# Kernel tuning notes

Measured on AMD Instinct MI355X. Metric: run time of the kernel, lower is better.

The kernel has to match this reference:

```python
import jax, jax.numpy as jnp
import numpy as np

N = 100000
E = 1600000
IN_C = 128
HID = 256
K_EIG = 64
OUT_C = 16


def setup_inputs() -> dict:
    key = jax.random.key(0)
    ks = jax.random.split(key, 8)
    x = jax.random.normal(ks[0], (N, IN_C), dtype=jnp.float32)
    edge_index = jax.random.randint(ks[1], (2, E), 0, N)
    MLP_W = jax.random.normal(ks[2], (K_EIG, N), dtype=jnp.float32) * 0.02
    MLP_b = jax.random.normal(ks[3], (K_EIG,), dtype=jnp.float32) * 0.02
    mlpx_W = jax.random.normal(ks[4], (HID, IN_C), dtype=jnp.float32) * 0.05
    mlpx_b = jax.random.normal(ks[5], (HID,), dtype=jnp.float32) * 0.02
    fin_W = jax.random.normal(ks[6], (OUT_C, HID + K_EIG), dtype=jnp.float32) * 0.05
    fin_b = jax.random.normal(ks[7], (OUT_C,), dtype=jnp.float32) * 0.02
    return {"x": x, "edge_index": edge_index, "MLP_W": MLP_W, "MLP_b": MLP_b,
            "mlpx_W": mlpx_W, "mlpx_b": mlpx_b, "fin_W": fin_W, "fin_b": fin_b}


def _spmm(row, col, feats, n):
    # adj is COO with coords (col[e], row[e]) and value 1 -> out[col] += feats[row]
    return jax.ops.segment_sum(feats[row], col, num_segments=n)


def _pump(xA, row, col, n):
    # MinCut-style pump: soft assignment, normalized-cut loss + orthogonality loss
    S = jax.nn.softmax(xA, axis=-1)                      # [N, K]
    AS = _spmm(row, col, S, n)                            # A @ S, [N, K]
    cut = jnp.sum(S * AS)                                 # tr(S^T A S)
    deg = jax.ops.segment_sum(jnp.ones(col.shape, S.dtype), col, num_segments=n)
    deg_term = jnp.sum(deg[:, None] * S * S)              # tr(S^T D S)
    pump_loss = -(cut / deg_term)
    SS = S.T @ S                                          # [K, K]
    k = S.shape[1]
    ortho_loss = jnp.linalg.norm(SS / jnp.linalg.norm(SS)
                                 - jnp.eye(k, dtype=S.dtype) / jnp.sqrt(jnp.asarray(k, S.dtype)))
    return S, pump_loss, ortho_loss


def reference(x, edge_index, MLP_W, MLP_b, mlpx_W, mlpx_b, fin_W, fin_b):
    row, col = edge_index[0], edge_index[1]
    n = x.shape[0]
    # xA = adj @ MLP.weight.T + bias   (irregular gather/scatter over edges)
    xA = _spmm(row, col, MLP_W.T, n) + MLP_b              # [N, K]
    xX = x @ mlpx_W.T + mlpx_b                            # [N, HID]
    xA, pump_loss, ortho_loss = _pump(xA, row, col, n)
    z = jnp.concatenate([xX, xA], axis=1)                 # [N, HID+K]
    # dropout omitted (eval mode)
    z = jax.nn.log_softmax(z @ fin_W.T + fin_b, axis=-1)  # [N, OUT]
    return (z, pump_loss + ortho_loss)
```

## Files before the change

### kernel.cpp

```cpp
#include <hip/hip_runtime.h>
#include <math.h>

#define N_NODES 100000
#define N_EDGES 1600000
#define IN_C    128
#define HID     256
#define KEIG    64
#define OUT_C   16

#define NPB      256
#define NBUCKET  ((N_NODES + NPB - 1) / NPB)
#define EDGE_TILE 4096
#define NTILE    ((N_EDGES + EDGE_TILE - 1) / EDGE_TILE)

#define TRANS_BLOCKS   ((N_NODES + 63) / 64)
#define GATHER_BLOCKS  2048
#define CUT_BLOCKS     2048
#define SSP_BLOCKS     512
#define OUT_BLOCKS     ((N_NODES + 255) / 256)

typedef __attribute__((ext_vector_type(8))) short short8;
typedef __attribute__((ext_vector_type(4))) float f32x4;

__device__ __forceinline__ float wave_sum(float v) {
#pragma unroll
    for (int m = 32; m; m >>= 1) v += __shfl_xor(v, m, 64);
    return v;
}
__device__ __forceinline__ float wave_max(float v) {
#pragma unroll
    for (int m = 32; m; m >>= 1) v = fmaxf(v, __shfl_xor(v, m, 64));
    return v;
}
__device__ __forceinline__ float bf2f(unsigned int u) {
    return __uint_as_float((u & 0xffffu) << 16);
}
__device__ __forceinline__ unsigned short f2bf(float f) {
    unsigned int u = __float_as_uint(f);
    u += 0x7fff + ((u >> 16) & 1);
    return (unsigned short)(u >> 16);
}

#define FMA4(P, s, W) \
    P.x = fmaf(s, W.x, P.x); P.y = fmaf(s, W.y, P.y); \
    P.z = fmaf(s, W.z, P.z); P.w = fmaf(s, W.w, P.w);

__global__ void prep_weff(const float* __restrict__ mlpxW, const float* __restrict__ mlpxb,
                          const float* __restrict__ finW, const float* __restrict__ finb,
                          float* __restrict__ Weff, float* __restrict__ beff,
                          int* __restrict__ bcnt) {
    int t = blockIdx.x * blockDim.x + threadIdx.x;
    const int NW = (IN_C + KEIG) * OUT_C;
    if (t < NW) {
        int k = t >> 4, o = t & 15;
        float acc;
        if (k < IN_C) {
            acc = 0.f;
            for (int c = 0; c < HID; ++c)
                acc += mlpxW[c * IN_C + k] * finW[o * (HID + KEIG) + c];
        } else {
            acc = finW[o * (HID + KEIG) + HID + (k - IN_C)];
        }
        Weff[k * OUT_C + o] = acc;
    }
    int tb = t - NW;
    if (tb >= 0 && tb < OUT_C) {
        float acc = finb[tb];
        for (int c = 0; c < HID; ++c) acc += mlpxb[c] * finW[tb * (HID + KEIG) + c];
        beff[tb] = acc;
    }
    int tz = t - (NW + OUT_C);
    if (tz >= 0 && tz <= NBUCKET) bcnt[tz] = 0;
}

__global__ void transpose_w(const float* __restrict__ W, unsigned short* __restrict__ WTb) {
    __shared__ float tile[64][65];
    int n0 = blockIdx.x * 64;
    int t = threadIdx.x;
    int tn = t & 63, tq = t >> 6;
#pragma unroll
    for (int kk = 0; kk < 16; ++kk) {
        int k = tq * 16 + kk;
        int n = n0 + tn;
        tile[k][tn] = (n < N_NODES) ? W[(long long)k * N_NODES + n] : 0.f;
    }
    __syncthreads();
    int tk = t & 63;
#pragma unroll
    for (int ii = 0; ii < 16; ++ii) {
        int n = n0 + tq * 16 + ii;
        if (n < N_NODES) WTb[(long long)n * 64 + tk] = f2bf(tile[tk][tq * 16 + ii]);
    }
}

__global__ void bucket_hist(const int* __restrict__ ei, int* __restrict__ bcnt) {
    __shared__ int h[NBUCKET];
    int t = threadIdx.x;
    for (int i = t; i < NBUCKET; i += 256) h[i] = 0;
    __syncthreads();
    int e0 = blockIdx.x * EDGE_TILE;
    int e1 = min(e0 + EDGE_TILE, N_EDGES);
    for (int e = e0 + t; e < e1; e += 256)
        atomicAdd(&h[ei[N_EDGES + e] >> 8], 1);
    __syncthreads();
    for (int i = t; i < NBUCKET; i += 256)
        if (h[i]) atomicAdd(&bcnt[i], h[i]);
}

__global__ void bucket_scan(const int* __restrict__ bcnt, int* __restrict__ bbase,
                            int* __restrict__ bcur) {
    __shared__ int sh[512];
    int t = threadIdx.x;
    int v = (t < NBUCKET) ? bcnt[t] : 0;
    sh[t] = v;
    __syncthreads();
    for (int d = 1; d < 512; d <<= 1) {
        int u = (t >= d) ? sh[t - d] : 0;
        __syncthreads();
        sh[t] += u;
        __syncthreads();
    }
    if (t < NBUCKET) { bbase[t] = sh[t] - v; bcur[t] = sh[t] - v; }
    if (t == 0) bbase[NBUCKET] = N_EDGES;
}

__global__ void bucket_scatter(const int* __restrict__ ei, int* __restrict__ bcur,
                               int* __restrict__ ebuf) {
    __shared__ int h[NBUCKET];
    __shared__ int gb[NBUCKET];
    int t = threadIdx.x;
    for (int i = t; i < NBUCKET; i += 256) h[i] = 0;
    __syncthreads();
    int e0 = blockIdx.x * EDGE_TILE;
    int e1 = min(e0 + EDGE_TILE, N_EDGES);
    for (int e = e0 + t; e < e1; e += 256)
        atomicAdd(&h[ei[N_EDGES + e] >> 8], 1);
    __syncthreads();
    for (int i = t; i < NBUCKET; i += 256) {
        int c = h[i];
        gb[i] = c ? atomicAdd(&bcur[i], c) : 0;
        h[i] = 0;
    }
    __syncthreads();
    for (int e = e0 + t; e < e1; e += 256) {
        int r = ei[e];
        int c = ei[N_EDGES + e];
        int b = c >> 8;
        int pos = gb[b] + atomicAdd(&h[b], 1);
        ebuf[pos] = r | ((c & 255) << 17);
    }
}

__global__ void csr_build(const int* __restrict__ ebuf, const int* __restrict__ bbase,
                          int* __restrict__ offsets, int* __restrict__ csr_row) {
    __shared__ int hist[NPB];
    __shared__ int sh[NPB];
    __shared__ int curs[NPB];
    int b = blockIdx.x;
    int t = threadIdx.x;
    int s0 = bbase[b], s1 = bbase[b + 1];
    hist[t] = 0;
    __syncthreads();
    for (int i = s0 + t; i < s1; i += 256)
        atomicAdd(&hist[ebuf[i] >> 17], 1);
    __syncthreads();
    int v = hist[t];
    sh[t] = v;
    __syncthreads();
    for (int d = 1; d < 256; d <<= 1) {
        int u = (t >= d) ? sh[t - d] : 0;
        __syncthreads();
        sh[t] += u;
        __syncthreads();
    }
    int excl = s0 + sh[t] - v;
    int node = b * NPB + t;
    if (node < N_NODES) offsets[node] = excl;
    curs[t] = excl;
    __syncthreads();
    for (int i = s0 + t; i < s1; i += 256) {
        int pk = ebuf[i];
        int pos = atomicAdd(&curs[pk >> 17], 1);
        csr_row[pos] = pk & 0x1FFFF;
    }
    if (b == 0 && t == 0) offsets[N_NODES] = N_EDGES;
}

__global__ void gather_softmax(const int* __restrict__ offsets, const int* __restrict__ csr_row,
                               const unsigned short* __restrict__ WTb,
                               const float* __restrict__ MLPb,
                               unsigned short* __restrict__ Sb,
                               float* __restrict__ dtp) {
    int lane = threadIdx.x & 63;
    int wib = threadIdx.x >> 6;
    int gw = (blockIdx.x * blockDim.x + threadIdx.x) >> 6;
    int nw = (gridDim.x * blockDim.x) >> 6;
    float bias = MLPb[lane];
    float dacc = 0.f;
    for (int n = gw; n < N_NODES; n += nw) {
        int s0 = offsets[n], s1 = offsets[n + 1];
        float acc = bias;
        for (int base = s0; base < s1; base += 64) {
            int cnt = min(64, s1 - base);
            int rv = (lane < cnt) ? csr_row[base + lane] : 0;
            int j = 0;
            for (; j + 3 < cnt; j += 4) {
                int r0 = __shfl(rv, j, 64);
                int r1 = __shfl(rv, j + 1, 64);
                int r2 = __shfl(rv, j + 2, 64);
                int r3 = __shfl(rv, j + 3, 64);
                float v0 = bf2f(WTb[(long long)r0 * 64 + lane]);
                float v1 = bf2f(WTb[(long long)r1 * 64 + lane]);
                float v2 = bf2f(WTb[(long long)r2 * 64 + lane]);
                float v3 = bf2f(WTb[(long long)r3 * 64 + lane]);
                acc += (v0 + v1) + (v2 + v3);
            }
            for (; j < cnt; ++j) {
                int r = __shfl(rv, j, 64);
                acc += bf2f(WTb[(long long)r * 64 + lane]);
            }
        }
        float m = wave_max(acc);
        float e = __expf(acc - m);
        float sm = wave_sum(e);
        float sv = e / sm;
        Sb[(long long)n * 64 + lane] = f2bf(sv);
        dacc += (float)(s1 - s0) * sv * sv;
    }
    dacc = wave_sum(dacc);
    __shared__ float red[4];
    if (lane == 0) red[wib] = dacc;
    __syncthreads();
    if (threadIdx.x == 0) dtp[blockIdx.x] = red[0] + red[1] + red[2] + red[3];
}

__global__ void cut_csr(const int* __restrict__ offsets, const int* __restrict__ csr_row,
                        const unsigned short* __restrict__ Sb, float* __restrict__ cutp) {
    int lane = threadIdx.x & 63;
    int wib = threadIdx.x >> 6;
    int gw = (blockIdx.x * blockDim.x + threadIdx.x) >> 6;
    int nw = (gridDim.x * blockDim.x) >> 6;
    float acc = 0.f;
    for (int n = gw; n < N_NODES; n += nw) {
        float sc = bf2f(Sb[(long long)n * 64 + lane]);
        int s0 = offsets[n], s1 = offsets[n + 1];
        float g = 0.f;
        for (int base = s0; base < s1; base += 64) {
            int cnt = min(64, s1 - base);
            int rv = (lane < cnt) ? csr_row[base + lane] : 0;
            int j = 0;
            for (; j + 3 < cnt; j += 4) {
                int r0 = __shfl(rv, j, 64);
                int r1 = __shfl(rv, j + 1, 64);
                int r2 = __shfl(rv, j + 2, 64);
                int r3 = __shfl(rv, j + 3, 64);
                float v0 = bf2f(Sb[(long long)r0 * 64 + lane]);
                float v1 = bf2f(Sb[(long long)r1 * 64 + lane]);
                float v2 = bf2f(Sb[(long long)r2 * 64 + lane]);
                float v3 = bf2f(Sb[(long long)r3 * 64 + lane]);
                g += (v0 + v1) + (v2 + v3);
            }
            for (; j < cnt; ++j) {
                int r = __shfl(rv, j, 64);
                g += bf2f(Sb[(long long)r * 64 + lane]);
            }
        }
        acc += sc * g;
    }
    acc = wave_sum(acc);
    __shared__ float red[4];
    if (lane == 0) red[wib] = acc;
    __syncthreads();
    if (threadIdx.x == 0) cutp[blockIdx.x] = red[0] + red[1] + red[2] + red[3];
}

__global__ __launch_bounds__(256) void ss_mfma(const unsigned short* __restrict__ Sb,
                                               float* __restrict__ ssp) {
    __shared__ unsigned short Sr[32][66];
    int t = threadIdx.x;
    int lane = t & 63;
    int w = t >> 6;
    int m = lane & 15;
    int quad = lane >> 4;
    int srow = t >> 3;
    int spart = t & 7;

    f32x4 a0 = {0.f,0.f,0.f,0.f}, a1 = {0.f,0.f,0.f,0.f};
    f32x4 a2 = {0.f,0.f,0.f,0.f}, a3 = {0.f,0.f,0.f,0.f};

    for (int base = blockIdx.x * 32; base < N_NODES; base += SSP_BLOCKS * 32) {
        const uint4* g = (const uint4*)(Sb + (long long)(base + srow) * 64 + spart * 8);
        uint4 d = *g;
        __syncthreads();
        unsigned int* rowp = (unsigned int*)&Sr[srow][0];
        rowp[spart * 4 + 0] = d.x;
        rowp[spart * 4 + 1] = d.y;
        rowp[spart * 4 + 2] = d.z;
        rowp[spart * 4 + 3] = d.w;
        __syncthreads();

        short8 f0, f1, f2, f3;
#pragma unroll
        for (int j = 0; j < 8; ++j) {
            int k = quad * 8 + j;
            f0[j] = (short)Sr[k][m];
            f1[j] = (short)Sr[k][16 + m];
            f2[j] = (short)Sr[k][32 + m];
            f3[j] = (short)Sr[k][48 + m];
        }
        short8 fa = (w == 0) ? f0 : (w == 1) ? f1 : (w == 2) ? f2 : f3;
        a0 = __builtin_amdgcn_mfma_f32_16x16x32_bf16(fa, f0, a0, 0, 0, 0);
        a1 = __builtin_amdgcn_mfma_f32_16x16x32_bf16(fa, f1, a1, 0, 0, 0);
        a2 = __builtin_amdgcn_mfma_f32_16x16x32_bf16(fa, f2, a2, 0, 0, 0);
        a3 = __builtin_amdgcn_mfma_f32_16x16x32_bf16(fa, f3, a3, 0, 0, 0);
    }

    float* dst = ssp + (size_t)blockIdx.x * 4096;
#pragma unroll
    for (int r = 0; r < 4; ++r) {
        int row = w * 16 + quad * 4 + r;
        dst[row * 64 +  0 + m] = a0[r];
        dst[row * 64 + 16 + m] = a1[r];
        dst[row * 64 + 32 + m] = a2[r];
        dst[row * 64 + 48 + m] = a3[r];
    }
}

__global__ void reduce_ss(const float* __restrict__ ssp, float* __restrict__ SS) {
    int e = blockIdx.x * blockDim.x + threadIdx.x;
    float s = 0.f;
    for (int p = 0; p < SSP_BLOCKS; ++p) s += ssp[(size_t)p * 4096 + e];
    SS[e] = s;
}

__global__ void scalars_kernel(const float* __restrict__ cutp, const float* __restrict__ dtp,
                               const float* __restrict__ SS, float* __restrict__ out) {
    __shared__ float red[256];
    int t = threadIdx.x;
    float c = 0.f;
    for (int i = t; i < CUT_BLOCKS; i += 256) c += cutp[i];
    red[t] = c; __syncthreads();
    for (int s = 128; s; s >>= 1) { if (t < s) red[t] += red[t + s]; __syncthreads(); }
    float cut = red[0]; __syncthreads();

    float d = 0.f;
    for (int i = t; i < GATHER_BLOCKS; i += 256) d += dtp[i];
    red[t] = d; __syncthreads();
    for (int s = 128; s; s >>= 1) { if (t < s) red[t] += red[t + s]; __syncthreads(); }
    float dterm = red[0]; __syncthreads();

    float ss[16];
    float sq = 0.f;
#pragma unroll
    for (int j = 0; j < 16; ++j) { ss[j] = SS[t * 16 + j]; sq += ss[j] * ss[j]; }
    red[t] = sq; __syncthreads();
    for (int s = 128; s; s >>= 1) { if (t < s) red[t] += red[t + s]; __syncthreads(); }
    float nrm = sqrtf(red[0]); __syncthreads();

    float osq = 0.f;
#pragma unroll
    for (int j = 0; j < 16; ++j) {
        int idx = t * 16 + j;
        float v = ss[j] / nrm - ((idx % 65 == 0) ? 0.125f : 0.f);
        osq += v * v;
    }
    red[t] = osq; __syncthreads();
    for (int s = 128; s; s >>= 1) { if (t < s) red[t] += red[t + s]; __syncthreads(); }
    if (t == 0) {
        float loss = -(cut / dterm) + sqrtf(red[0]);
        out[(long long)N_NODES * OUT_C] = loss;
    }
}

__global__ __launch_bounds__(256) void out_kernel(const float* __restrict__ x,
                           const unsigned short* __restrict__ Sb,
                           const float* __restrict__ Weff, const float* __restrict__ beff,
                           float* __restrict__ out) {
    __shared__ float4 Wsh[192 * 4];
    __shared__ float bsh[16];
    int t = threadIdx.x;
    const float4* W4 = (const float4*)Weff;
    for (int i = t; i < 768; i += 256) Wsh[i] = W4[i];
    if (t < 16) bsh[t] = beff[t];
    __syncthreads();

    int r = blockIdx.x * 256 + t;
    if (r >= N_NODES) return;

    float4 p0 = make_float4(bsh[0], bsh[1], bsh[2], bsh[3]);
    float4 p1 = make_float4(bsh[4], bsh[5], bsh[6], bsh[7]);
    float4 p2 = make_float4(bsh[8], bsh[9], bsh[10], bsh[11]);
    float4 p3 = make_float4(bsh[12], bsh[13], bsh[14], bsh[15]);

    const float4* xr = (const float4*)(x + (long long)r * IN_C);
#pragma unroll 8
    for (int j = 0; j < 32; ++j) {
        float4 xv = xr[j];
        int k = j * 4;
        float xs[4] = {xv.x, xv.y, xv.z, xv.w};
#pragma unroll
        for (int c = 0; c < 4; ++c) {
            float s = xs[c];
            float4 w0 = Wsh[(k + c) * 4 + 0];
            float4 w1 = Wsh[(k + c) * 4 + 1];
            float4 w2 = Wsh[(k + c) * 4 + 2];
            float4 w3 = Wsh[(k + c) * 4 + 3];
            FMA4(p0, s, w0); FMA4(p1, s, w1); FMA4(p2, s, w2); FMA4(p3, s, w3);
        }
    }
    const uint2* sr = (const uint2*)(Sb + (long long)r * 64);
#pragma unroll 8
    for (int j = 0; j < 16; ++j) {
        uint2 u = sr[j];
        float xs[4] = {bf2f(u.x), bf2f(u.x >> 16), bf2f(u.y), bf2f(u.y >> 16)};
        int k = IN_C + j * 4;
#pragma unroll
        for (int c = 0; c < 4; ++c) {
            float s = xs[c];
            float4 w0 = Wsh[(k + c) * 4 + 0];
            float4 w1 = Wsh[(k + c) * 4 + 1];
            float4 w2 = Wsh[(k + c) * 4 + 2];
            float4 w3 = Wsh[(k + c) * 4 + 3];
            FMA4(p0, s, w0); FMA4(p1, s, w1); FMA4(p2, s, w2); FMA4(p3, s, w3);
        }
    }

    float m = fmaxf(fmaxf(fmaxf(p0.x, p0.y), fmaxf(p0.z, p0.w)),
                    fmaxf(fmaxf(fmaxf(p1.x, p1.y), fmaxf(p1.z, p1.w)),
                          fmaxf(fmaxf(fmaxf(p2.x, p2.y), fmaxf(p2.z, p2.w)),
                                fmaxf(fmaxf(p3.x, p3.y), fmaxf(p3.z, p3.w)))));
    float sum = __expf(p0.x - m) + __expf(p0.y - m) + __expf(p0.z - m) + __expf(p0.w - m)
              + __expf(p1.x - m) + __expf(p1.y - m) + __expf(p1.z - m) + __expf(p1.w - m)
              + __expf(p2.x - m) + __expf(p2.y - m) + __expf(p2.z - m) + __expf(p2.w - m)
              + __expf(p3.x - m) + __expf(p3.y - m) + __expf(p3.z - m) + __expf(p3.w - m);
    float lse = m + logf(sum);
    float4* o4 = (float4*)(out + (long long)r * OUT_C);
    o4[0] = make_float4(p0.x - lse, p0.y - lse, p0.z - lse, p0.w - lse);
    o4[1] = make_float4(p1.x - lse, p1.y - lse, p1.z - lse, p1.w - lse);
    o4[2] = make_float4(p2.x - lse, p2.y - lse, p2.z - lse, p2.w - lse);
    o4[3] = make_float4(p3.x - lse, p3.y - lse, p3.z - lse, p3.w - lse);
}

extern "C" void kernel_launch(void* const* d_in, const int* in_sizes, int n_in,
                              void* d_out, int out_size, void* d_ws, size_t ws_size,
                              hipStream_t stream) {
    const float* x     = (const float*)d_in[0];
    const int*   ei    = (const int*)d_in[1];
    const float* MLPW  = (const float*)d_in[2];
    const float* MLPb  = (const float*)d_in[3];
    const float* mlpxW = (const float*)d_in[4];
    const float* mlpxb = (const float*)d_in[5];
    const float* finW  = (const float*)d_in[6];
    const float* finb  = (const float*)d_in[7];
    float* out = (float*)d_out;
    float* ws  = (float*)d_ws;

    unsigned short* WTb = (unsigned short*)ws;
    unsigned short* Sb  = (unsigned short*)(ws + (size_t)N_NODES * 32);
    float* ssp  = ws + (size_t)N_NODES * 64;
    float* SS   = ssp + (size_t)SSP_BLOCKS * 4096;
    float* Weff = SS + 4096;
    float* beff = Weff + 192 * 16;
    float* cutp = beff + 16;
    float* dtp  = cutp + CUT_BLOCKS;
    int* ebuf    = (int*)(dtp + GATHER_BLOCKS);
    int* csr_row = ebuf + N_EDGES;
    int* offsets = csr_row + N_EDGES;
    int* bcnt    = offsets + N_NODES + 1;
    int* bbase   = bcnt + NBUCKET + 1;
    int* bcur    = bbase + NBUCKET + 1;

    hipLaunchKernelGGL(prep_weff, dim3(14), dim3(256), 0, stream,
                       mlpxW, mlpxb, finW, finb, Weff, beff, bcnt);
    hipLaunchKernelGGL(transpose_w, dim3(TRANS_BLOCKS), dim3(256), 0, stream, MLPW, WTb);
    hipLaunchKernelGGL(bucket_hist, dim3(NTILE), dim3(256), 0, stream, ei, bcnt);
    hipLaunchKernelGGL(bucket_scan, dim3(1), dim3(512), 0, stream, bcnt, bbase, bcur);
    hipLaunchKernelGGL(bucket_scatter, dim3(NTILE), dim3(256), 0, stream, ei, bcur, ebuf);
    hipLaunchKernelGGL(csr_build, dim3(NBUCKET), dim3(256), 0, stream,
                       ebuf, bbase, offsets, csr_row);
    hipLaunchKernelGGL(gather_softmax, dim3(GATHER_BLOCKS), dim3(256), 0, stream,
                       offsets, csr_row, WTb, MLPb, Sb, dtp);
    hipLaunchKernelGGL(cut_csr, dim3(CUT_BLOCKS), dim3(256), 0, stream,
                       offsets, csr_row, Sb, cutp);
    hipLaunchKernelGGL(ss_mfma, dim3(SSP_BLOCKS), dim3(256), 0, stream, Sb, ssp);
    hipLaunchKernelGGL(reduce_ss, dim3(16), dim3(256), 0, stream, ssp, SS);
    hipLaunchKernelGGL(scalars_kernel, dim3(1), dim3(256), 0, stream, cutp, dtp, SS, out);
    hipLaunchKernelGGL(out_kernel, dim3(OUT_BLOCKS), dim3(256), 0, stream, x, Sb, Weff, beff, out);
}
```

Baseline: 335.6 us.

## Gather fp8 half-feature tables in two passes for L2-resident gathers

Stores the transposed MLP weight and the softmax assignments as scaled fp8 and splits each 64-wide feature into two 32-byte halves. The sparse gathers then run as two passes over the CSR, each touching a 3.2 MB table that can stay cache-resident, with the two half-waves covering alternating edges. The aim is to cut the random-gather bytes and cache misses of the SpMM and the cut computation. In exchange, the CSR indices are traversed twice, there is an extra fp32 intermediate buffer, and fp8 quantization lowers accuracy of xA and the cut term.

```diff
diff --git a/kernel.cpp b/kernel.cpp
--- a/kernel.cpp
+++ b/kernel.cpp
@@ -39,6 +39,13 @@
     unsigned int u = __float_as_uint(f);
     u += 0x7fff + ((u >> 16) & 1);
     return (unsigned short)(u >> 16);
+}
+__device__ __forceinline__ float fp8tof(int b) {
+    return __builtin_amdgcn_cvt_f32_fp8(b, 0);
+}
+__device__ __forceinline__ unsigned char f2fp8(float f) {
+    int p = __builtin_amdgcn_cvt_pk_fp8_f32(f, f, 0, false);
+    return (unsigned char)(p & 0xff);
 }
 
 #define FMA4(P, s, W) \
@@ -73,7 +80,8 @@
     if (tz >= 0 && tz <= NBUCKET) bcnt[tz] = 0;
 }
 
-__global__ void transpose_w(const float* __restrict__ W, unsigned short* __restrict__ WTb) {
+__global__ void transpose_w(const float* __restrict__ W, unsigned char* __restrict__ WT8a,
+                            unsigned char* __restrict__ WT8b) {
     __shared__ float tile[64][65];
     int n0 = blockIdx.x * 64;
     int t = threadIdx.x;
@@ -89,7 +97,11 @@
 #pragma unroll
     for (int ii = 0; ii < 16; ++ii) {
         int n = n0 + tq * 16 + ii;
-        if (n < N_NODES) WTb[(long long)n * 64 + tk] = f2bf(tile[tk][tq * 16 + ii]);
+        if (n < N_NODES) {
+            unsigned char v = f2fp8(tile[tk][tq * 16 + ii] * 32.f);
+            if (tk < 32) WT8a[(unsigned)n * 32u + tk] = v;
+            else         WT8b[(unsigned)n * 32u + (tk - 32)] = v;
+        }
     }
 }
 
@@ -186,12 +198,47 @@
     if (b == 0 && t == 0) offsets[N_NODES] = N_EDGES;
 }
 
+__global__ void gather_phaseA(const int* __restrict__ offsets, const int* __restrict__ csr_row,
+                              const unsigned char* __restrict__ WT8a,
+                              float* __restrict__ xAa) {
+    int lane = threadIdx.x & 63;
+    int sub = lane >> 5, kk = lane & 31;
+    int gw = (blockIdx.x * blockDim.x + threadIdx.x) >> 6;
+    int nw = (gridDim.x * blockDim.x) >> 6;
+    for (int n = gw; n < N_NODES; n += nw) {
+        int s0 = offsets[n], s1 = offsets[n + 1];
+        float acc = 0.f;
+        for (int base = s0; base < s1; base += 64) {
+            int cnt = min(64, s1 - base);
+            int rv = (lane < cnt) ? csr_row[base + lane] : 0;
+            int cm1 = cnt - 1;
+            for (int pb = 0; pb * 2 < cnt; pb += 8) {
+                float vs = 0.f;
+#pragma unroll
+                for (int q = 0; q < 8; ++q) {
+                    int j = (pb + q) * 2 + sub;
+                    int r = __shfl(rv, min(j, cm1), 64);
+                    int b = WT8a[(unsigned)r * 32u + kk];
+                    vs += (j <= cm1) ? fp8tof(b) : 0.f;
+                }
+                acc += vs;
+            }
+        }
+        acc += __shfl_xor(acc, 32, 64);
+        if (lane < 32) xAa[(unsigned)n * 32u + kk] = acc;
+    }
+}
+
 __global__ void gather_softmax(const int* __restrict__ offsets, const int* __restrict__ csr_row,
-                               const unsigned short* __restrict__ WTb,
+                               const unsigned char* __restrict__ WT8b,
+                               const float* __restrict__ xAa,
                                const float* __restrict__ MLPb,
                                unsigned short* __restrict__ Sb,
+                               unsigned char* __restrict__ S8a,
+                               unsigned char* __restrict__ S8b,
                                float* __restrict__ dtp) {
     int lane = threadIdx.x & 63;
+    int sub = lane >> 5, kk = lane & 31;
     int wib = threadIdx.x >> 6;
     int gw = (blockIdx.x * blockDim.x + threadIdx.x) >> 6;
     int nw = (gridDim.x * blockDim.x) >> 6;
@@ -199,32 +246,34 @@
     float dacc = 0.f;
     for (int n = gw; n < N_NODES; n += nw) {
         int s0 = offsets[n], s1 = offsets[n + 1];
-        float acc = bias;
+        float acc = 0.f;
         for (int base = s0; base < s1; base += 64) {
             int cnt = min(64, s1 - base);
             int rv = (lane < cnt) ? csr_row[base + lane] : 0;
-            int j = 0;
-            for (; j + 3 < cnt; j += 4) {
-                int r0 = __shfl(rv, j, 64);
-                int r1 = __shfl(rv, j + 1, 64);
-                int r2 = __shfl(rv, j + 2, 64);
-                int r3 = __shfl(rv, j + 3, 64);
-                float v0 = bf2f(WTb[(long long)r0 * 64 + lane]);
-                float v1 = bf2f(WTb[(long long)r1 * 64 + lane]);
-                float v2 = bf2f(WTb[(long long)r2 * 64 + lane]);
-                float v3 = bf2f(WTb[(long long)r3 * 64 + lane]);
-                acc += (v0 + v1) + (v2 + v3);
+            int cm1 = cnt - 1;
+            for (int pb = 0; pb * 2 < cnt; pb += 8) {
+                float vs = 0.f;
+#pragma unroll
+                for (int q = 0; q < 8; ++q) {
+                    int j = (pb + q) * 2 + sub;
+                    int r = __shfl(rv, min(j, cm1), 64);
+                    int b = WT8b[(unsigned)r * 32u + kk];
+                    vs += (j <= cm1) ? fp8tof(b) : 0.f;
+                }
+                acc += vs;
             }
-            for (; j < cnt; ++j) {
-                int r = __shfl(rv, j, 64);
-                acc += bf2f(WTb[(long long)r * 64 + lane]);
-            }
-        }
-        float m = wave_max(acc);
-        float e = __expf(acc - m);
+        }
+        float foldB = acc + __shfl_xor(acc, 32, 64);
+        float xa = xAa[(unsigned)n * 32u + kk];
+        float full = bias + ((sub == 0) ? xa : foldB) * 0.03125f;
+        float m = wave_max(full);
+        float e = __expf(full - m);
         float sm = wave_sum(e);
         float sv = e / sm;
-        Sb[(long long)n * 64 + lane] = f2bf(sv);
+        Sb[(unsigned)n * 64u + lane] = f2bf(sv);
+        unsigned char s8 = f2fp8(sv * 64.f);
+        if (sub == 0) S8a[(unsigned)n * 32u + kk] = s8;
+        else          S8b[(unsigned)n * 32u + kk] = s8;
         dacc += (float)(s1 - s0) * sv * sv;
     }
     dacc = wave_sum(dacc);
@@ -234,40 +283,39 @@
     if (threadIdx.x == 0) dtp[blockIdx.x] = red[0] + red[1] + red[2] + red[3];
 }
 
-__global__ void cut_csr(const int* __restrict__ offsets, const int* __restrict__ csr_row,
-                        const unsigned short* __restrict__ Sb, float* __restrict__ cutp) {
+__global__ void cut_phase(const int* __restrict__ offsets, const int* __restrict__ csr_row,
+                          const unsigned short* __restrict__ Sb,
+                          const unsigned char* __restrict__ S8h, int koff,
+                          float* __restrict__ cutp) {
     int lane = threadIdx.x & 63;
+    int sub = lane >> 5, kk = lane & 31;
     int wib = threadIdx.x >> 6;
     int gw = (blockIdx.x * blockDim.x + threadIdx.x) >> 6;
     int nw = (gridDim.x * blockDim.x) >> 6;
     float acc = 0.f;
     for (int n = gw; n < N_NODES; n += nw) {
-        float sc = bf2f(Sb[(long long)n * 64 + lane]);
+        float sc = bf2f(Sb[(unsigned)n * 64u + koff + kk]);
         int s0 = offsets[n], s1 = offsets[n + 1];
         float g = 0.f;
         for (int base = s0; base < s1; base += 64) {
             int cnt = min(64, s1 - base);
             int rv = (lane < cnt) ? csr_row[base + lane] : 0;
-            int j = 0;
-            for (; j + 3 < cnt; j += 4) {
-                int r0 = __shfl(rv, j, 64);
-                int r1 = __shfl(rv, j + 1, 64);
-                int r2 = __shfl(rv, j + 2, 64);
-                int r3 = __shfl(rv, j + 3, 64);
-                float v0 = bf2f(Sb[(long long)r0 * 64 + lane]);
-                float v1 = bf2f(Sb[(long long)r1 * 64 + lane]);
-                float v2 = bf2f(Sb[(long long)r2 * 64 + lane]);
-                float v3 = bf2f(Sb[(long long)r3 * 64 + lane]);
-                g += (v0 + v1) + (v2 + v3);
+            int cm1 = cnt - 1;
+            for (int pb = 0; pb * 2 < cnt; pb += 8) {
+                float vs = 0.f;
+#pragma unroll
+                for (int q = 0; q < 8; ++q) {
+                    int j = (pb + q) * 2 + sub;
+                    int r = __shfl(rv, min(j, cm1), 64);
+                    int b = S8h[(unsigned)r * 32u + kk];
+                    vs += (j <= cm1) ? fp8tof(b) : 0.f;
+                }
+                g += vs;
             }
-            for (; j < cnt; ++j) {
-                int r = __shfl(rv, j, 64);
-                g += bf2f(Sb[(long long)r * 64 + lane]);
-            }
         }
         acc += sc * g;
     }
-    acc = wave_sum(acc);
+    acc = wave_sum(acc) * 0.015625f;
     __shared__ float red[4];
     if (lane == 0) red[wib] = acc;
     __syncthreads();
@@ -338,7 +386,7 @@
     __shared__ float red[256];
     int t = threadIdx.x;
     float c = 0.f;
-    for (int i = t; i < CUT_BLOCKS; i += 256) c += cutp[i];
+    for (int i = t; i < 2 * CUT_BLOCKS; i += 256) c += cutp[i];
     red[t] = c; __syncthreads();
     for (int s = 128; s; s >>= 1) { if (t < s) red[t] += red[t + s]; __syncthreads(); }
     float cut = red[0]; __syncthreads();
@@ -453,16 +501,20 @@
     const float* finW  = (const float*)d_in[6];
     const float* finb  = (const float*)d_in[7];
     float* out = (float*)d_out;
-    float* ws  = (float*)d_ws;
-
-    unsigned short* WTb = (unsigned short*)ws;
-    unsigned short* Sb  = (unsigned short*)(ws + (size_t)N_NODES * 32);
-    float* ssp  = ws + (size_t)N_NODES * 64;
+    char* ws = (char*)d_ws;
+
+    unsigned char*  WT8a = (unsigned char*)ws;
+    unsigned char*  WT8b = (unsigned char*)(ws + (size_t)N_NODES * 32);
+    unsigned char*  S8a  = (unsigned char*)(ws + (size_t)N_NODES * 64);
+    unsigned char*  S8b  = (unsigned char*)(ws + (size_t)N_NODES * 96);
+    unsigned short* Sb   = (unsigned short*)(ws + (size_t)N_NODES * 128);
+    float* xAa  = (float*)(ws + (size_t)N_NODES * 256);
+    float* ssp  = (float*)(ws + (size_t)N_NODES * 384);
     float* SS   = ssp + (size_t)SSP_BLOCKS * 4096;
     float* Weff = SS + 4096;
     float* beff = Weff + 192 * 16;
     float* cutp = beff + 16;
-    float* dtp  = cutp + CUT_BLOCKS;
+    float* dtp  = cutp + 2 * CUT_BLOCKS;
     int* ebuf    = (int*)(dtp + GATHER_BLOCKS);
     int* csr_row = ebuf + N_EDGES;
     int* offsets = csr_row + N_EDGES;
@@ -472,16 +524,21 @@
 
     hipLaunchKernelGGL(prep_weff, dim3(14), dim3(256), 0, stream,
                        mlpxW, mlpxb, finW, finb, Weff, beff, bcnt);
-    hipLaunchKernelGGL(transpose_w, dim3(TRANS_BLOCKS), dim3(256), 0, stream, MLPW, WTb);
+    hipLaunchKernelGGL(transpose_w, dim3(TRANS_BLOCKS), dim3(256), 0, stream,
+                       MLPW, WT8a, WT8b);
     hipLaunchKernelGGL(bucket_hist, dim3(NTILE), dim3(256), 0, stream, ei, bcnt);
     hipLaunchKernelGGL(bucket_scan, dim3(1), dim3(512), 0, stream, bcnt, bbase, bcur);
     hipLaunchKernelGGL(bucket_scatter, dim3(NTILE), dim3(256), 0, stream, ei, bcur, ebuf);
     hipLaunchKernelGGL(csr_build, dim3(NBUCKET), dim3(256), 0, stream,
                        ebuf, bbase, offsets, csr_row);
+    hipLaunchKernelGGL(gather_phaseA, dim3(GATHER_BLOCKS), dim3(256), 0, stream,
+                       offsets, csr_row, WT8a, xAa);
     hipLaunchKernelGGL(gather_softmax, dim3(GATHER_BLOCKS), dim3(256), 0, stream,
-                       offsets, csr_row, WTb, MLPb, Sb, dtp);
-    hipLaunchKernelGGL(cut_csr, dim3(CUT_BLOCKS), dim3(256), 0, stream,
-                       offsets, csr_row, Sb, cutp);
+                       offsets, csr_row, WT8b, xAa, MLPb, Sb, S8a, S8b, dtp);
+    hipLaunchKernelGGL(cut_phase, dim3(CUT_BLOCKS), dim3(256), 0, stream,
+                       offsets, csr_row, Sb, S8a, 0, cutp);
+    hipLaunchKernelGGL(cut_phase, dim3(CUT_BLOCKS), dim3(256), 0, stream,
+                       offsets, csr_row, Sb, S8b, 32, cutp + CUT_BLOCKS);
     hipLaunchKernelGGL(ss_mfma, dim3(SSP_BLOCKS), dim3(256), 0, stream, Sb, ssp);
     hipLaunchKernelGGL(reduce_ss, dim3(16), dim3(256), 0, stream, ssp, SS);
     hipLaunchKernelGGL(scalars_kernel, dim3(1), dim3(256), 0, stream, cutp, dtp, SS, out);
```

Measured after the change: 455.3 us. 35.6% more time.
